# Performance work log

Hardware: AMD Instinct MI355X
Metric: run time of the kernel (lower is better)

Reference implementation:

```python
import jax, jax.numpy as jnp
import numpy as np

N_NODES = 50000
N_EDGES = 800000
NDIM_IN = 64
EDIM = 64
NDIM_OUT = [128, 128]


def setup_inputs() -> dict:
    key = jax.random.key(0)
    ks = jax.random.split(key, 12)
    inp = {
        "nfeats": jax.random.normal(ks[0], (N_NODES, 1, NDIM_IN), dtype=jnp.float32),
        "efeats": jax.random.normal(ks[1], (N_EDGES, 1, EDIM), dtype=jnp.float32),
        "dst": jax.random.randint(ks[2], (N_EDGES,), 0, N_NODES, dtype=jnp.int32),
    }
    # Layer 0 MLP: Linear(ndim_in+edim -> 128), ReLU, Linear(128 -> 128), ReLU
    d0_in = NDIM_IN + EDIM
    s = 1.0 / np.sqrt(d0_in)
    inp["W1_0"] = jax.random.uniform(ks[3], (d0_in, NDIM_OUT[0]), jnp.float32, -s, s)
    inp["b1_0"] = jax.random.uniform(ks[4], (NDIM_OUT[0],), jnp.float32, -s, s)
    s = 1.0 / np.sqrt(NDIM_OUT[0])
    inp["W2_0"] = jax.random.uniform(ks[5], (NDIM_OUT[0], NDIM_OUT[0]), jnp.float32, -s, s)
    inp["b2_0"] = jax.random.uniform(ks[6], (NDIM_OUT[0],), jnp.float32, -s, s)
    # Layer 1 MLP: Linear(128+edim -> 128), ReLU, Linear(128 -> 128), ReLU
    d1_in = NDIM_OUT[0] + EDIM
    s = 1.0 / np.sqrt(d1_in)
    inp["W1_1"] = jax.random.uniform(ks[7], (d1_in, NDIM_OUT[1]), jnp.float32, -s, s)
    inp["b1_1"] = jax.random.uniform(ks[8], (NDIM_OUT[1],), jnp.float32, -s, s)
    s = 1.0 / np.sqrt(NDIM_OUT[1])
    inp["W2_1"] = jax.random.uniform(ks[9], (NDIM_OUT[1], NDIM_OUT[1]), jnp.float32, -s, s)
    inp["b2_1"] = jax.random.uniform(ks[10], (NDIM_OUT[1],), jnp.float32, -s, s)
    return inp


def _gin_layer(h, h_neigh, W1, b1, W2, b2):
    # concat node state with scatter-summed edge features, then 2-layer MLP
    x = jnp.concatenate([h, h_neigh], axis=-1)  # [N, 1, d_in + edim]
    x = jax.nn.relu(x @ W1 + b1)
    return jax.nn.relu(x @ W2 + b2)


def reference(nfeats, efeats, dst,
              W1_0, b1_0, W2_0, b2_0,
              W1_1, b1_1, W2_1, b2_1):
    n = nfeats.shape[0]
    # update_all(copy_e, sum): scatter-add edge features onto destination nodes.
    # efeats never changes (edge_update path disabled), so h_neigh is layer-invariant.
    h_neigh = jax.ops.segment_sum(efeats, dst, num_segments=n)  # [N, 1, edim]
    h = _gin_layer(nfeats, h_neigh, W1_0, b1_0, W2_0, b2_0)
    # dropout is identity in eval mode (deterministic reference)
    h = _gin_layer(h, h_neigh, W1_1, b1_1, W2_1, b2_1)
    return h.sum(axis=1)  # [N, ndim_out[-1]]
```

## Files before the change

### kernel.cpp

```cpp
#include <hip/hip_runtime.h>
#include <hip/hip_bf16.h>

#define N_NODES 50000
#define N_EDGES 800000
#define EDIM 64
#define NT 64
#define XS 200
#define NTILES 782
#define NSUB 16
#define SCAP 128
#define TCAP (NSUB * SCAP)

#define FP_SCALE 2097152.0f
#define FP_INV   (1.0f / 2097152.0f)

typedef __attribute__((ext_vector_type(8))) short  bf16x8_t;
typedef __attribute__((ext_vector_type(4))) short  bf16x4_t;
typedef __attribute__((ext_vector_type(4))) float  f32x4_t;

__device__ __forceinline__ unsigned short f2bf(float f) {
    unsigned u = __float_as_uint(f);
    unsigned r = u + 0x7fff + ((u >> 16) & 1);
    return (unsigned short)(r >> 16);
}
__device__ __forceinline__ float bf2f(unsigned short s) {
    return __uint_as_float(((unsigned)s) << 16);
}

__global__ __launch_bounds__(256) void prep_bucket_kernel(
    const float* __restrict__ W1_0, const float* __restrict__ W2_0,
    const float* __restrict__ W1_1, const float* __restrict__ W2_1,
    unsigned short* __restrict__ wbuf,
    const int* __restrict__ dst, int* __restrict__ cnt, int* __restrict__ bucket)
{
    int bid = blockIdx.x, t = threadIdx.x;

    if (bid >= 288) {
        int i = (bid - 288) * 256 + t;
        if (i < N_EDGES / 4) {
            int4 d = ((const int4*)dst)[i];
            int e0 = i * 4;
            int sub = t & (NSUB - 1);
            int t0 = d.x >> 6, t1 = d.y >> 6, t2 = d.z >> 6, t3 = d.w >> 6;
            int p0 = atomicAdd(&cnt[t0 * NSUB + sub], 1);
            int p1 = atomicAdd(&cnt[t1 * NSUB + sub], 1);
            int p2 = atomicAdd(&cnt[t2 * NSUB + sub], 1);
            int p3 = atomicAdd(&cnt[t3 * NSUB + sub], 1);
            if (p0 < SCAP) bucket[t0 * TCAP + sub * SCAP + p0] = (e0    ) | ((d.x & 63) << 20);
            if (p1 < SCAP) bucket[t1 * TCAP + sub * SCAP + p1] = (e0 + 1) | ((d.y & 63) << 20);
            if (p2 < SCAP) bucket[t2 * TCAP + sub * SCAP + p2] = (e0 + 2) | ((d.z & 63) << 20);
            if (p3 < SCAP) bucket[t3 * TCAP + sub * SCAP + p3] = (e0 + 3) | ((d.w & 63) << 20);
        }
        return;
    }

    const float* W; unsigned short *whi, *wlo; int K, idx;
    if (bid < 64)       { W = W1_0; K = 128; whi = wbuf;          wlo = wbuf + 16384;  idx = bid * 256 + t; }
    else if (bid < 128) { W = W2_0; K = 128; whi = wbuf + 32768;  wlo = wbuf + 49152;  idx = (bid - 64) * 256 + t; }
    else if (bid < 224) { W = W1_1; K = 192; whi = wbuf + 65536;  wlo = wbuf + 90112;  idx = (bid - 128) * 256 + t; }
    else                { W = W2_1; K = 128; whi = wbuf + 114688; wlo = wbuf + 131072; idx = (bid - 224) * 256 + t; }
    int k = idx >> 7, n = idx & 127;
    float w = W[idx];
    unsigned short h = f2bf(w);
    unsigned short l = f2bf(w - bf2f(h));
    whi[n * K + k] = h;
    wlo[n * K + k] = l;
}


template <int KTOT, bool FINAL>
__device__ __forceinline__ void mfma_linear(short* Xhi, short* Xlo,
    const unsigned short* __restrict__ whi, const unsigned short* __restrict__ wlo,
    const float* __restrict__ bias, float* __restrict__ out, int node0, int t)
{
    const int lane = t & 63, wv = t >> 6, quad = lane >> 4, l15 = lane & 15;
    const int chb = wv * 32;

    f32x4_t acc[4][2];
    #pragma unroll
    for (int mt = 0; mt < 4; ++mt) {
        acc[mt][0] = (f32x4_t){0.f, 0.f, 0.f, 0.f};
        acc[mt][1] = (f32x4_t){0.f, 0.f, 0.f, 0.f};
    }
    float bv0 = bias[chb + l15];
    float bv1 = bias[chb + 16 + l15];

    const unsigned short* w0h = whi + (size_t)(chb + l15) * KTOT;
    const unsigned short* w0l = wlo + (size_t)(chb + l15) * KTOT;
    const unsigned short* w1h = whi + (size_t)(chb + 16 + l15) * KTOT;
    const unsigned short* w1l = wlo + (size_t)(chb + 16 + l15) * KTOT;

    #pragma unroll
    for (int ks = 0; ks < KTOT / 32; ++ks) {
        int kk = ks * 32 + quad * 8;
        bf16x8_t b0h = *(const bf16x8_t*)(w0h + kk);
        bf16x8_t b0l = *(const bf16x8_t*)(w0l + kk);
        bf16x8_t b1h = *(const bf16x8_t*)(w1h + kk);
        bf16x8_t b1l = *(const bf16x8_t*)(w1l + kk);
        #pragma unroll
        for (int mt = 0; mt < 4; ++mt) {
            bf16x8_t ah = *(const bf16x8_t*)(&Xhi[(mt * 16 + l15) * XS + kk]);
            bf16x8_t al = *(const bf16x8_t*)(&Xlo[(mt * 16 + l15) * XS + kk]);
            acc[mt][0] = __builtin_amdgcn_mfma_f32_16x16x32_bf16(ah, b0h, acc[mt][0], 0, 0, 0);
            acc[mt][0] = __builtin_amdgcn_mfma_f32_16x16x32_bf16(al, b0h, acc[mt][0], 0, 0, 0);
            acc[mt][0] = __builtin_amdgcn_mfma_f32_16x16x32_bf16(ah, b0l, acc[mt][0], 0, 0, 0);
            acc[mt][1] = __builtin_amdgcn_mfma_f32_16x16x32_bf16(ah, b1h, acc[mt][1], 0, 0, 0);
            acc[mt][1] = __builtin_amdgcn_mfma_f32_16x16x32_bf16(al, b1h, acc[mt][1], 0, 0, 0);
            acc[mt][1] = __builtin_amdgcn_mfma_f32_16x16x32_bf16(ah, b1l, acc[mt][1], 0, 0, 0);
        }
    }

    __syncthreads();

    if (!FINAL) {
        #pragma unroll
        for (int mt = 0; mt < 4; ++mt) {
            #pragma unroll
            for (int nt = 0; nt < 2; ++nt) {
                float bb = nt ? bv1 : bv0;
                int ch = chb + nt * 16 + l15;
                #pragma unroll
                for (int r = 0; r < 4; ++r) {
                    float y = fmaxf(acc[mt][nt][r] + bb, 0.f);
                    unsigned short h = f2bf(y);
                    unsigned short l = f2bf(y - bf2f(h));
                    int m = mt * 16 + quad * 4 + r;
                    Xhi[m * XS + ch] = (short)h;
                    Xlo[m * XS + ch] = (short)l;
                }
            }
        }
        __syncthreads();
    } else {
        #pragma unroll
        for (int mt = 0; mt < 4; ++mt) {
            #pragma unroll
            for (int nt = 0; nt < 2; ++nt) {
                float bb = nt ? bv1 : bv0;
                int ch = chb + nt * 16 + l15;
                #pragma unroll
                for (int r = 0; r < 4; ++r) {
                    int gn = node0 + mt * 16 + quad * 4 + r;
                    if (gn < N_NODES)
                        out[(size_t)gn * 128 + ch] = fmaxf(acc[mt][nt][r] + bb, 0.f);
                }
            }
        }
    }
}

__global__ __launch_bounds__(256) void gin_fused_kernel(
    const float* __restrict__ nfeats, const float* __restrict__ efeats,
    const int* __restrict__ cnt, const int* __restrict__ bucket,
    const unsigned short* __restrict__ wbuf,
    const float* __restrict__ b1_0, const float* __restrict__ b2_0,
    const float* __restrict__ b1_1, const float* __restrict__ b2_1,
    float* __restrict__ out)
{
    __shared__ short Xhi[NT * XS];
    __shared__ short Xlo[NT * XS];
    int* acc = (int*)Xhi;

    const int t = threadIdx.x;
    const int tile = blockIdx.x;
    const int node0 = tile * NT;
    const int wv = t >> 6, lane = t & 63;

    float4 nf[4];
    #pragma unroll
    for (int rep = 0; rep < 4; ++rep) {
        int idx = rep * 256 + t;
        int node = idx >> 4, kq = idx & 15;
        int gn = node0 + node;
        nf[rep] = make_float4(0.f, 0.f, 0.f, 0.f);
        if (gn < N_NODES) nf[rep] = *(const float4*)(nfeats + (size_t)gn * 64 + kq * 4);
    }

    #pragma unroll
    for (int i = t; i < NT * 64; i += 256) acc[i] = 0;
    __syncthreads();

    const int* cbase = cnt + tile * NSUB;
    for (int si = 0; si < 4; ++si) {
        int s = (wv << 2) + si;
        int ms = cbase[s];
        const int* blist = bucket + tile * TCAP + s * SCAP;
        for (int base = 0; base < ms; base += 8) {
            int pk[8];
            #pragma unroll
            for (int k = 0; k < 8; ++k) {
                int j = base + k;
                pk[k] = blist[(j < ms) ? j : (ms - 1)];
            }
            float v[8];
            #pragma unroll
            for (int k = 0; k < 8; ++k)
                v[k] = __builtin_nontemporal_load(efeats + (size_t)(pk[k] & 0xFFFFF) * 64 + lane);
            #pragma unroll
            for (int k = 0; k < 8; ++k) {
                if (base + k < ms)
                    atomicAdd(&acc[((pk[k] >> 20) << 6) + lane], __float2int_rn(v[k] * FP_SCALE));
            }
        }
    }
    __syncthreads();

    int4 av[4];
    #pragma unroll
    for (int rep = 0; rep < 4; ++rep) {
        int idx = rep * 256 + t;
        int node = idx >> 4, kq = idx & 15;
        av[rep] = *(const int4*)(acc + node * 64 + kq * 4);
    }
    __syncthreads();

    #pragma unroll
    for (int rep = 0; rep < 4; ++rep) {
        int idx = rep * 256 + t;
        int node = idx >> 4, kq = idx & 15;
        {
            float4 v = nf[rep];
            unsigned short h0 = f2bf(v.x), h1 = f2bf(v.y), h2 = f2bf(v.z), h3 = f2bf(v.w);
            bf16x4_t hv = {(short)h0, (short)h1, (short)h2, (short)h3};
            bf16x4_t lv = {(short)f2bf(v.x - bf2f(h0)), (short)f2bf(v.y - bf2f(h1)),
                           (short)f2bf(v.z - bf2f(h2)), (short)f2bf(v.w - bf2f(h3))};
            *(bf16x4_t*)(&Xhi[node * XS + kq * 4]) = hv;
            *(bf16x4_t*)(&Xlo[node * XS + kq * 4]) = lv;
        }
        {
            float4 v = make_float4(av[rep].x * FP_INV, av[rep].y * FP_INV,
                                   av[rep].z * FP_INV, av[rep].w * FP_INV);
            unsigned short h0 = f2bf(v.x), h1 = f2bf(v.y), h2 = f2bf(v.z), h3 = f2bf(v.w);
            bf16x4_t hv = {(short)h0, (short)h1, (short)h2, (short)h3};
            bf16x4_t lv = {(short)f2bf(v.x - bf2f(h0)), (short)f2bf(v.y - bf2f(h1)),
                           (short)f2bf(v.z - bf2f(h2)), (short)f2bf(v.w - bf2f(h3))};
            int r0 = node * XS + 64  + kq * 4;
            int r1 = node * XS + 128 + kq * 4;
            *(bf16x4_t*)(&Xhi[r0]) = hv;
            *(bf16x4_t*)(&Xlo[r0]) = lv;
            *(bf16x4_t*)(&Xhi[r1]) = hv;
            *(bf16x4_t*)(&Xlo[r1]) = lv;
        }
    }
    __syncthreads();

    mfma_linear<128, false>(Xhi, Xlo, wbuf,          wbuf + 16384,  b1_0, nullptr, node0, t);
    mfma_linear<128, false>(Xhi, Xlo, wbuf + 32768,  wbuf + 49152,  b2_0, nullptr, node0, t);
    mfma_linear<192, false>(Xhi, Xlo, wbuf + 65536,  wbuf + 90112,  b1_1, nullptr, node0, t);
    mfma_linear<128, true >(Xhi, Xlo, wbuf + 114688, wbuf + 131072, b2_1, out,     node0, t);
}

extern "C" void kernel_launch(void* const* d_in, const int* in_sizes, int n_in,
                              void* d_out, int out_size, void* d_ws, size_t ws_size,
                              hipStream_t stream)
{
    const float* nfeats = (const float*)d_in[0];
    const float* efeats = (const float*)d_in[1];
    const int*   dst    = (const int*)d_in[2];
    const float* W1_0   = (const float*)d_in[3];
    const float* b1_0   = (const float*)d_in[4];
    const float* W2_0   = (const float*)d_in[5];
    const float* b2_0   = (const float*)d_in[6];
    const float* W1_1   = (const float*)d_in[7];
    const float* b1_1   = (const float*)d_in[8];
    const float* W2_1   = (const float*)d_in[9];
    const float* b2_1   = (const float*)d_in[10];
    float* out = (float*)d_out;

    char* ws = (char*)d_ws;
    int*            cnt    = (int*)ws;
    int*            bucket = (int*)(ws + 50176);
    unsigned short* wbuf   = (unsigned short*)(ws + 6456320);

    hipMemsetAsync(cnt, 0, NTILES * NSUB * sizeof(int), stream);

    prep_bucket_kernel<<<288 + NTILES, 256, 0, stream>>>(
        W1_0, W2_0, W1_1, W2_1, wbuf, dst, cnt, bucket);

    gin_fused_kernel<<<NTILES, 256, 0, stream>>>(
        nfeats, efeats, cnt, bucket, wbuf, b1_0, b2_0, b1_1, b2_1, out);
}
```

Baseline: 486.5 us.

## Split fused gather+MLP kernel into separate gather and MFMA MLP kernels

Moves the edge-feature scatter-sum into its own kernel that uses only 16KB of LDS and launch bounds allowing 8 blocks per CU, writing fixed-point sums to a global workspace. The MLP kernel then reads those sums and nfeats to stage the bf16 hi/lo operands. The aim is more blocks in flight during the latency-bound gather, which the fused kernel's large LDS footprint limited. The cost is an extra global round trip of about 12.8MB and an additional kernel launch.

```diff
diff --git a/kernel.cpp b/kernel.cpp
--- a/kernel.cpp
+++ b/kernel.cpp
@@ -67,6 +67,100 @@
     wlo[n * K + k] = l;
 }
 
+__global__ __launch_bounds__(256, 8) void gather_kernel(
+    const float* __restrict__ efeats,
+    const int* __restrict__ cnt, const int* __restrict__ bucket,
+    int* __restrict__ hn)
+{
+    __shared__ int acc[NT * 64];
+    const int t = threadIdx.x;
+    const int tile = blockIdx.x;
+    const int wv = t >> 6, lane = t & 63;
+
+    #pragma unroll
+    for (int i = t; i < NT * 64; i += 256) acc[i] = 0;
+    __syncthreads();
+
+    const int* cbase = cnt + tile * NSUB;
+    for (int si = 0; si < 4; ++si) {
+        int s = (wv << 2) + si;
+        int ms = cbase[s];
+        const int* blist = bucket + tile * TCAP + s * SCAP;
+        for (int base = 0; base < ms; base += 8) {
+            int pk[8];
+            #pragma unroll
+            for (int k = 0; k < 8; ++k) {
+                int j = base + k;
+                pk[k] = blist[(j < ms) ? j : (ms - 1)];
+            }
+            float v[8];
+            #pragma unroll
+            for (int k = 0; k < 8; ++k)
+                v[k] = __builtin_nontemporal_load(efeats + (size_t)(pk[k] & 0xFFFFF) * 64 + lane);
+            #pragma unroll
+            for (int k = 0; k < 8; ++k) {
+                if (base + k < ms)
+                    atomicAdd(&acc[((pk[k] >> 20) << 6) + lane], __float2int_rn(v[k] * FP_SCALE));
+            }
+        }
+    }
+    __syncthreads();
+
+    int4* d4 = (int4*)(hn + (size_t)tile * NT * 64);
+    const int4* s4 = (const int4*)acc;
+    #pragma unroll
+    for (int r = 0; r < 4; ++r) d4[r * 256 + t] = s4[r * 256 + t];
+}
+
+
+__device__ __forceinline__ void stage_x(short* Xhi, short* Xlo,
+                                        const float* __restrict__ g,
+                                        int node0, int k0, int t)
+{
+    #pragma unroll
+    for (int rep = 0; rep < 4; ++rep) {
+        int idx  = rep * 256 + t;
+        int node = idx >> 4;
+        int kq   = idx & 15;
+        int gn   = node0 + node;
+        float4 v = make_float4(0.f, 0.f, 0.f, 0.f);
+        if (gn < N_NODES) v = *(const float4*)(g + (size_t)gn * 64 + kq * 4);
+        unsigned short h0 = f2bf(v.x), h1 = f2bf(v.y), h2 = f2bf(v.z), h3 = f2bf(v.w);
+        bf16x4_t hv = {(short)h0, (short)h1, (short)h2, (short)h3};
+        bf16x4_t lv = {(short)f2bf(v.x - bf2f(h0)), (short)f2bf(v.y - bf2f(h1)),
+                       (short)f2bf(v.z - bf2f(h2)), (short)f2bf(v.w - bf2f(h3))};
+        *(bf16x4_t*)(&Xhi[node * XS + k0 + kq * 4]) = hv;
+        *(bf16x4_t*)(&Xlo[node * XS + k0 + kq * 4]) = lv;
+    }
+}
+
+__device__ __forceinline__ void stage_hn(short* Xhi, short* Xlo,
+                                         const int* __restrict__ g,
+                                         int node0, int t)
+{
+    #pragma unroll
+    for (int rep = 0; rep < 4; ++rep) {
+        int idx  = rep * 256 + t;
+        int node = idx >> 4;
+        int kq   = idx & 15;
+        int gn   = node0 + node;
+        float4 v = make_float4(0.f, 0.f, 0.f, 0.f);
+        if (gn < N_NODES) {
+            int4 iv = *(const int4*)(g + (size_t)gn * 64 + kq * 4);
+            v = make_float4(iv.x * FP_INV, iv.y * FP_INV, iv.z * FP_INV, iv.w * FP_INV);
+        }
+        unsigned short h0 = f2bf(v.x), h1 = f2bf(v.y), h2 = f2bf(v.z), h3 = f2bf(v.w);
+        bf16x4_t hv = {(short)h0, (short)h1, (short)h2, (short)h3};
+        bf16x4_t lv = {(short)f2bf(v.x - bf2f(h0)), (short)f2bf(v.y - bf2f(h1)),
+                       (short)f2bf(v.z - bf2f(h2)), (short)f2bf(v.w - bf2f(h3))};
+        int r0 = node * XS + 64 + kq * 4;
+        int r1 = node * XS + 128 + kq * 4;
+        *(bf16x4_t*)(&Xhi[r0]) = hv;
+        *(bf16x4_t*)(&Xlo[r0]) = lv;
+        *(bf16x4_t*)(&Xhi[r1]) = hv;
+        *(bf16x4_t*)(&Xlo[r1]) = lv;
+    }
+}
 
 template <int KTOT, bool FINAL>
 __device__ __forceinline__ void mfma_linear(short* Xhi, short* Xlo,
@@ -149,9 +243,8 @@
     }
 }
 
-__global__ __launch_bounds__(256) void gin_fused_kernel(
-    const float* __restrict__ nfeats, const float* __restrict__ efeats,
-    const int* __restrict__ cnt, const int* __restrict__ bucket,
+__global__ __launch_bounds__(256) void gin_mlp_mfma_kernel(
+    const float* __restrict__ nfeats, const int* __restrict__ hn_int,
     const unsigned short* __restrict__ wbuf,
     const float* __restrict__ b1_0, const float* __restrict__ b2_0,
     const float* __restrict__ b1_1, const float* __restrict__ b2_1,
@@ -159,89 +252,11 @@
 {
     __shared__ short Xhi[NT * XS];
     __shared__ short Xlo[NT * XS];
-    int* acc = (int*)Xhi;
-
     const int t = threadIdx.x;
-    const int tile = blockIdx.x;
-    const int node0 = tile * NT;
-    const int wv = t >> 6, lane = t & 63;
-
-    float4 nf[4];
-    #pragma unroll
-    for (int rep = 0; rep < 4; ++rep) {
-        int idx = rep * 256 + t;
-        int node = idx >> 4, kq = idx & 15;
-        int gn = node0 + node;
-        nf[rep] = make_float4(0.f, 0.f, 0.f, 0.f);
-        if (gn < N_NODES) nf[rep] = *(const float4*)(nfeats + (size_t)gn * 64 + kq * 4);
-    }
-
-    #pragma unroll
-    for (int i = t; i < NT * 64; i += 256) acc[i] = 0;
-    __syncthreads();
-
-    const int* cbase = cnt + tile * NSUB;
-    for (int si = 0; si < 4; ++si) {
-        int s = (wv << 2) + si;
-        int ms = cbase[s];
-        const int* blist = bucket + tile * TCAP + s * SCAP;
-        for (int base = 0; base < ms; base += 8) {
-            int pk[8];
-            #pragma unroll
-            for (int k = 0; k < 8; ++k) {
-                int j = base + k;
-                pk[k] = blist[(j < ms) ? j : (ms - 1)];
-            }
-            float v[8];
-            #pragma unroll
-            for (int k = 0; k < 8; ++k)
-                v[k] = __builtin_nontemporal_load(efeats + (size_t)(pk[k] & 0xFFFFF) * 64 + lane);
-            #pragma unroll
-            for (int k = 0; k < 8; ++k) {
-                if (base + k < ms)
-                    atomicAdd(&acc[((pk[k] >> 20) << 6) + lane], __float2int_rn(v[k] * FP_SCALE));
-            }
-        }
-    }
-    __syncthreads();
-
-    int4 av[4];
-    #pragma unroll
-    for (int rep = 0; rep < 4; ++rep) {
-        int idx = rep * 256 + t;
-        int node = idx >> 4, kq = idx & 15;
-        av[rep] = *(const int4*)(acc + node * 64 + kq * 4);
-    }
-    __syncthreads();
-
-    #pragma unroll
-    for (int rep = 0; rep < 4; ++rep) {
-        int idx = rep * 256 + t;
-        int node = idx >> 4, kq = idx & 15;
-        {
-            float4 v = nf[rep];
-            unsigned short h0 = f2bf(v.x), h1 = f2bf(v.y), h2 = f2bf(v.z), h3 = f2bf(v.w);
-            bf16x4_t hv = {(short)h0, (short)h1, (short)h2, (short)h3};
-            bf16x4_t lv = {(short)f2bf(v.x - bf2f(h0)), (short)f2bf(v.y - bf2f(h1)),
-                           (short)f2bf(v.z - bf2f(h2)), (short)f2bf(v.w - bf2f(h3))};
-            *(bf16x4_t*)(&Xhi[node * XS + kq * 4]) = hv;
-            *(bf16x4_t*)(&Xlo[node * XS + kq * 4]) = lv;
-        }
-        {
-            float4 v = make_float4(av[rep].x * FP_INV, av[rep].y * FP_INV,
-                                   av[rep].z * FP_INV, av[rep].w * FP_INV);
-            unsigned short h0 = f2bf(v.x), h1 = f2bf(v.y), h2 = f2bf(v.z), h3 = f2bf(v.w);
-            bf16x4_t hv = {(short)h0, (short)h1, (short)h2, (short)h3};
-            bf16x4_t lv = {(short)f2bf(v.x - bf2f(h0)), (short)f2bf(v.y - bf2f(h1)),
-                           (short)f2bf(v.z - bf2f(h2)), (short)f2bf(v.w - bf2f(h3))};
-            int r0 = node * XS + 64  + kq * 4;
-            int r1 = node * XS + 128 + kq * 4;
-            *(bf16x4_t*)(&Xhi[r0]) = hv;
-            *(bf16x4_t*)(&Xlo[r0]) = lv;
-            *(bf16x4_t*)(&Xhi[r1]) = hv;
-            *(bf16x4_t*)(&Xlo[r1]) = lv;
-        }
-    }
+    const int node0 = blockIdx.x * NT;
+
+    stage_x(Xhi, Xlo, nfeats, node0, 0, t);
+    stage_hn(Xhi, Xlo, hn_int, node0, t);
     __syncthreads();
 
     mfma_linear<128, false>(Xhi, Xlo, wbuf,          wbuf + 16384,  b1_0, nullptr, node0, t);
@@ -268,15 +283,18 @@
     float* out = (float*)d_out;
 
     char* ws = (char*)d_ws;
-    int*            cnt    = (int*)ws;
-    int*            bucket = (int*)(ws + 50176);
-    unsigned short* wbuf   = (unsigned short*)(ws + 6456320);
+    int*            hn_int = (int*)ws;
+    int*            cnt    = (int*)(ws + 12812288);
+    int*            bucket = (int*)(ws + 12863488);
+    unsigned short* wbuf   = (unsigned short*)(ws + 19269632);
 
     hipMemsetAsync(cnt, 0, NTILES * NSUB * sizeof(int), stream);
 
     prep_bucket_kernel<<<288 + NTILES, 256, 0, stream>>>(
         W1_0, W2_0, W1_1, W2_1, wbuf, dst, cnt, bucket);
 
-    gin_fused_kernel<<<NTILES, 256, 0, stream>>>(
-        nfeats, efeats, cnt, bucket, wbuf, b1_0, b2_0, b1_1, b2_1, out);
-}
+    gather_kernel<<<NTILES, 256, 0, stream>>>(efeats, cnt, bucket, hn_int);
+
+    gin_mlp_mfma_kernel<<<NTILES, 256, 0, stream>>>(
+        nfeats, hn_int, wbuf, b1_0, b2_0, b1_1, b2_1, out);
+}
```

New measurement: 441.7 us. 9.2% less time.
